# Kernel tuning notes

Measured on AMD Instinct MI355X. Metric: run time of the kernel, lower is better.

The kernel has to match this reference:

```python
import jax, jax.numpy as jnp
import numpy as np

B, N, C, F = 8, 2048, 256, 128

def setup_inputs() -> dict:
    key = jax.random.key(0)
    ks = jax.random.split(key, 5)
    s = 0.02
    return {
        "x": jax.random.normal(ks[0], (B, N, C), dtype=jnp.float32),
        "Wf": jax.random.normal(ks[1], (C, F), dtype=jnp.float32) * s,
        "bf": jnp.zeros((F,), jnp.float32),
        "Wg": jax.random.normal(ks[2], (C, F), dtype=jnp.float32) * s,
        "bg": jnp.zeros((F,), jnp.float32),
        "Wh": jax.random.normal(ks[3], (C, F), dtype=jnp.float32) * s,
        "bh": jnp.zeros((F,), jnp.float32),
        "Wv": jax.random.normal(ks[4], (F, F), dtype=jnp.float32) * s,
        "bv": jnp.zeros((F,), jnp.float32),
    }

def reference(x, Wf, bf, Wg, bg, Wh, bh, Wv, bv):
    # 1x1 Conv1D == pointwise dense projection
    fx = x @ Wf + bf            # [B, N, F]
    gx = x @ Wg + bg            # [B, N, F]
    hx = x @ Wh + bh            # [B, N, F]
    # alpha = softmax(fx @ gx^T) over last axis -> [B, N, N]
    alpha = jax.nn.softmax(jnp.einsum('bnf,bmf->bnm', fx, gx), axis=-1)
    # o = hx^T @ alpha -> [B, F, N]
    o = jnp.einsum('bnf,bnm->bfm', hx, alpha)
    # faithful to original: RESHAPE (not transpose) to [B, N, F]
    o = o.reshape(B, N, F)
    return o @ Wv + bv          # [B, N, F]
```

## Files before the change

kernel.cpp:

```cpp
#include <hip/hip_runtime.h>
#include <hip/hip_bf16.h>


constexpr int Bb = 8, Nn = 2048, Cc = 256, Ff = 128;
constexpr long BNF = (long)Bb * Nn * Ff;
constexpr long BN  = (long)Bb * Nn;

typedef __bf16 bf16x8 __attribute__((ext_vector_type(8)));
typedef float  f32x4  __attribute__((ext_vector_type(4)));

__device__ inline unsigned short f2bf(float x) {
    unsigned u = __float_as_uint(x);
    unsigned r = (u + 0x7fffu + ((u >> 16) & 1u)) >> 16;
    return (unsigned short)r;
}
__device__ inline float bf2f(unsigned short h) {
    return __uint_as_float(((unsigned)h) << 16);
}


__global__ __launch_bounds__(256) void k_prepw(
    const float* __restrict__ W0, const float* __restrict__ W1,
    const float* __restrict__ W2,
    ushort* __restrict__ wth, ushort* __restrict__ wtl)
{
    __shared__ float ls[64][132];
    const float* W = (blockIdx.y == 0) ? W0 : (blockIdx.y == 1) ? W1 : W2;
    const int k0 = blockIdx.x * 64;
    const int t = threadIdx.x;
    const float4* src = (const float4*)(W + (size_t)k0 * 128);
    #pragma unroll
    for (int i = 0; i < 8; ++i) {
        int idx = t + 256 * i;
        int r = idx >> 5, c4 = idx & 31;
        *(float4*)&ls[r][c4 * 4] = src[idx];
    }
    __syncthreads();
    const int f = t >> 1, half = t & 1;
    __align__(16) ushort hb[32], lb[32];
    #pragma unroll
    for (int j = 0; j < 32; ++j) {
        float v = ls[half * 32 + j][f];
        ushort h = f2bf(v);
        hb[j] = h;
        lb[j] = f2bf(v - bf2f(h));
    }
    size_t base = ((size_t)blockIdx.y * 128 + f) * 256 + k0 + half * 32;
    #pragma unroll
    for (int j = 0; j < 4; ++j) {
        *(uint4*)&wth[base + j * 8] = *(const uint4*)&hb[j * 8];
        *(uint4*)&wtl[base + j * 8] = *(const uint4*)&lb[j * 8];
    }
}

__global__ __launch_bounds__(256) void k_prepwv(
    const float* __restrict__ Wv,
    ushort* __restrict__ wvth, ushort* __restrict__ wvtl)
{
    __shared__ float ls[64][132];
    const int k0 = blockIdx.x * 64;
    const int t = threadIdx.x;
    const float4* src = (const float4*)(Wv + (size_t)k0 * 128);
    #pragma unroll
    for (int i = 0; i < 8; ++i) {
        int idx = t + 256 * i;
        int r = idx >> 5, c4 = idx & 31;
        *(float4*)&ls[r][c4 * 4] = src[idx];
    }
    __syncthreads();
    const int f = t >> 1, half = t & 1;
    __align__(16) ushort hb[32], lb[32];
    #pragma unroll
    for (int j = 0; j < 32; ++j) {
        float v = ls[half * 32 + j][f];
        ushort h = f2bf(v);
        hb[j] = h;
        lb[j] = f2bf(v - bf2f(h));
    }
    size_t base = (size_t)f * 128 + k0 + half * 32;
    #pragma unroll
    for (int j = 0; j < 4; ++j) {
        *(uint4*)&wvth[base + j * 8] = *(const uint4*)&hb[j * 8];
        *(uint4*)&wvtl[base + j * 8] = *(const uint4*)&lb[j * 8];
    }
}

__global__ __launch_bounds__(512) void k_projm2(
    const float* __restrict__ x,
    const ushort* __restrict__ wth, const ushort* __restrict__ wtl,
    const float* __restrict__ b0, const float* __restrict__ b1,
    const float* __restrict__ b2,
    ushort* __restrict__ fxh, ushort* __restrict__ fxl,
    ushort* __restrict__ gxh, ushort* __restrict__ gxl,
    float* __restrict__ hxt)
{
    __shared__ ushort xsh[64][264], xsl[64][264];
    __shared__ float pmf[64][132];
    ushort (*pm)[136] = (ushort(*)[136])pmf;

    const int t = threadIdx.x;
    const long row0 = (long)blockIdx.x * 64;
    const int wid = t >> 6, lane = t & 63;
    const int wy = wid & 1, wx = wid >> 1;
    const int col = lane & 15, quad = lane >> 4;

    {
        #pragma unroll
        for (int i = 0; i < 8; ++i) {
            int idx = t + 512 * i;
            int r = idx >> 6, c4 = idx & 63;
            float4 v = *(const float4*)&x[(row0 + r) * 256 + c4 * 4];
            ushort4 h, l;
            h.x = f2bf(v.x); l.x = f2bf(v.x - bf2f(h.x));
            h.y = f2bf(v.y); l.y = f2bf(v.y - bf2f(h.y));
            h.z = f2bf(v.z); l.z = f2bf(v.z - bf2f(h.z));
            h.w = f2bf(v.w); l.w = f2bf(v.w - bf2f(h.w));
            *(ushort4*)&xsh[r][c4 * 4] = h;
            *(ushort4*)&xsl[r][c4 * 4] = l;
        }
    }
    __syncthreads();

    for (int y = 0; y < 3; ++y) {
        const ushort* Wh = wth + (size_t)y * 128 * 256;
        const ushort* Wl = wtl + (size_t)y * 128 * 256;
        const float* bias = (y == 0) ? b0 : (y == 1) ? b1 : b2;

        f32x4 acc[2][2];
        #pragma unroll
        for (int i = 0; i < 2; ++i)
            #pragma unroll
            for (int j = 0; j < 2; ++j) acc[i][j] = (f32x4){0.f, 0.f, 0.f, 0.f};

        #pragma unroll
        for (int kk = 0; kk < 8; ++kk) {
            const int ko = kk * 32 + quad * 8;
            bf16x8 ah[2], al[2], bh[2], bl[2];
            #pragma unroll
            for (int tn = 0; tn < 2; ++tn) {
                int r = wy * 32 + tn * 16 + col;
                ah[tn] = *(const bf16x8*)&xsh[r][ko];
                al[tn] = *(const bf16x8*)&xsl[r][ko];
            }
            #pragma unroll
            for (int tf = 0; tf < 2; ++tf) {
                int f = wx * 32 + tf * 16 + col;
                bh[tf] = *(const bf16x8*)&Wh[(size_t)f * 256 + ko];
                bl[tf] = *(const bf16x8*)&Wl[(size_t)f * 256 + ko];
            }
            #pragma unroll
            for (int tn = 0; tn < 2; ++tn)
                #pragma unroll
                for (int tf = 0; tf < 2; ++tf) {
                    acc[tn][tf] = __builtin_amdgcn_mfma_f32_16x16x32_bf16(ah[tn], bh[tf], acc[tn][tf], 0, 0, 0);
                    acc[tn][tf] = __builtin_amdgcn_mfma_f32_16x16x32_bf16(ah[tn], bl[tf], acc[tn][tf], 0, 0, 0);
                    acc[tn][tf] = __builtin_amdgcn_mfma_f32_16x16x32_bf16(al[tn], bh[tf], acc[tn][tf], 0, 0, 0);
                }
        }

        float v[2][2][4];
        #pragma unroll
        for (int tf = 0; tf < 2; ++tf) {
            float bb = bias[wx * 32 + tf * 16 + col];
            #pragma unroll
            for (int tn = 0; tn < 2; ++tn)
                #pragma unroll
                for (int r = 0; r < 4; ++r) v[tn][tf][r] = acc[tn][tf][r] + bb;
        }

        if (y == 2) {
            float* ob = hxt + (row0 >> 11) * (size_t)128 * 2048;
            int n0 = (int)(row0 & 2047);
            #pragma unroll
            for (int tn = 0; tn < 2; ++tn) {
                int n = n0 + wy * 32 + tn * 16 + quad * 4;
                #pragma unroll
                for (int tf = 0; tf < 2; ++tf) {
                    int f = wx * 32 + tf * 16 + col;
                    f32x4 vv = {v[tn][tf][0], v[tn][tf][1], v[tn][tf][2], v[tn][tf][3]};
                    *(f32x4*)&ob[(size_t)f * 2048 + n] = vv;
                }
            }
        } else {
            ushort* oh = (y == 0) ? fxh : gxh;
            ushort* ol = (y == 0) ? fxl : gxl;
            __syncthreads();
            #pragma unroll
            for (int tn = 0; tn < 2; ++tn)
                #pragma unroll
                for (int tf = 0; tf < 2; ++tf)
                    #pragma unroll
                    for (int r = 0; r < 4; ++r)
                        pm[wy * 32 + tn * 16 + quad * 4 + r][wx * 32 + tf * 16 + col] = f2bf(v[tn][tf][r]);
            __syncthreads();
            #pragma unroll
            for (int i = 0; i < 2; ++i) {
                int idx = t + 512 * i;
                int r = idx >> 4, c = idx & 15;
                *(uint4*)&oh[(row0 + r) * 128 + c * 8] = *(const uint4*)&pm[r][c * 8];
            }
            __syncthreads();
            #pragma unroll
            for (int tn = 0; tn < 2; ++tn)
                #pragma unroll
                for (int tf = 0; tf < 2; ++tf)
                    #pragma unroll
                    for (int r = 0; r < 4; ++r) {
                        float hv = bf2f(f2bf(v[tn][tf][r]));
                        pm[wy * 32 + tn * 16 + quad * 4 + r][wx * 32 + tf * 16 + col] = f2bf(v[tn][tf][r] - hv);
                    }
            __syncthreads();
            #pragma unroll
            for (int i = 0; i < 2; ++i) {
                int idx = t + 512 * i;
                int r = idx >> 4, c = idx & 15;
                *(uint4*)&ol[(row0 + r) * 128 + c * 8] = *(const uint4*)&pm[r][c * 8];
            }
            __syncthreads();
        }
    }
}

__global__ __launch_bounds__(512, 4) void k_score5(
    const ushort* __restrict__ fxh, const ushort* __restrict__ fxl,
    const ushort* __restrict__ gxh, const ushort* __restrict__ gxl,
    ushort* __restrict__ Pt, float* __restrict__ lsum2)
{
    __shared__ ushort gsh[64][136], gsl[64][136];
    __shared__ __align__(16) ushort fsbuf[2 * 64 * 136];
    __shared__ float lsum[64];
    ushort* fsh = fsbuf;
    ushort* fsl = fsbuf + 64 * 136;
    ushort* pm  = fsbuf;

    const int t = threadIdx.x;
    const int n0g = blockIdx.x * 64;
    const int ms = blockIdx.y;
    const int b = n0g >> 11;
    const int n0 = n0g & 2047;
    const int wid = t >> 6, lane = t & 63;
    const int wy = wid & 1, wx = wid >> 1;
    const int col = lane & 15, quad = lane >> 4;

    {
        const uint4* sh = (const uint4*)(fxh + (size_t)n0g * 128);
        const uint4* sl = (const uint4*)(fxl + (size_t)n0g * 128);
        #pragma unroll
        for (int i = 0; i < 2; ++i) {
            int idx = t + 512 * i;
            int r = idx >> 4, c = idx & 15;
            *(uint4*)&fsh[r * 136 + c * 8] = sh[idx];
            *(uint4*)&fsl[r * 136 + c * 8] = sl[idx];
        }
        if (t < 64) lsum[t] = 0.f;
    }
    __syncthreads();

    bf16x8 Ah[4][2], Al[4][2];
    #pragma unroll
    for (int kk = 0; kk < 4; ++kk) {
        const int ko = kk * 32 + quad * 8;
        #pragma unroll
        for (int tn = 0; tn < 2; ++tn) {
            int r = wy * 32 + tn * 16 + col;
            Ah[kk][tn] = *(const bf16x8*)&fsh[r * 136 + ko];
            Al[kk][tn] = *(const bf16x8*)&fsl[r * 136 + ko];
        }
    }

    float rs[2][4] = {};
    const ushort* gbh = gxh + (size_t)b * 2048 * 128;
    const ushort* gbl = gxl + (size_t)b * 2048 * 128;
    ushort* Pb = Pt + (size_t)b * 2048 * 2048;

    for (int mt = 0; mt < 16; ++mt) {
        const int m0 = ms * 1024 + mt * 64;
        __syncthreads();
        {
            const uint4* sh = (const uint4*)(gbh + (size_t)m0 * 128);
            const uint4* sl = (const uint4*)(gbl + (size_t)m0 * 128);
            #pragma unroll
            for (int i = 0; i < 2; ++i) {
                int idx = t + 512 * i;
                int r = idx >> 4, c = idx & 15;
                *(uint4*)&gsh[r][c * 8] = sh[idx];
                *(uint4*)&gsl[r][c * 8] = sl[idx];
            }
        }
        __syncthreads();

        f32x4 acc[2];
        acc[0] = (f32x4){0.f, 0.f, 0.f, 0.f};
        acc[1] = (f32x4){0.f, 0.f, 0.f, 0.f};

        #pragma unroll
        for (int kk = 0; kk < 4; ++kk) {
            const int ko = kk * 32 + quad * 8;
            int r = wx * 16 + col;
            bf16x8 bh = *(const bf16x8*)&gsh[r][ko];
            bf16x8 bl = *(const bf16x8*)&gsl[r][ko];
            #pragma unroll
            for (int tn = 0; tn < 2; ++tn) {
                acc[tn] = __builtin_amdgcn_mfma_f32_16x16x32_bf16(Ah[kk][tn], bh, acc[tn], 0, 0, 0);
                acc[tn] = __builtin_amdgcn_mfma_f32_16x16x32_bf16(Ah[kk][tn], bl, acc[tn], 0, 0, 0);
                acc[tn] = __builtin_amdgcn_mfma_f32_16x16x32_bf16(Al[kk][tn], bh, acc[tn], 0, 0, 0);
            }
        }

        #pragma unroll
        for (int tn = 0; tn < 2; ++tn) {
            float e0 = __expf(acc[tn][0]);
            float e1 = __expf(acc[tn][1]);
            float e2 = __expf(acc[tn][2]);
            float e3 = __expf(acc[tn][3]);
            rs[tn][0] += e0; rs[tn][1] += e1; rs[tn][2] += e2; rs[tn][3] += e3;
            ushort4 pk;
            pk.x = f2bf(e0); pk.y = f2bf(e1); pk.z = f2bf(e2); pk.w = f2bf(e3);
            int ml = wx * 16 + col;
            int nl = wy * 32 + tn * 16 + quad * 4;
            *(ushort4*)&pm[ml * 72 + nl] = pk;
        }
        __syncthreads();
        {
            int r = t >> 3, c = t & 7;
            *(uint4*)&Pb[(size_t)(m0 + r) * 2048 + n0 + c * 8] = *(const uint4*)&pm[r * 72 + c * 8];
        }
    }

    #pragma unroll
    for (int off = 1; off < 16; off <<= 1)
        #pragma unroll
        for (int tn = 0; tn < 2; ++tn)
            #pragma unroll
            for (int r = 0; r < 4; ++r) rs[tn][r] += __shfl_xor(rs[tn][r], off);
    if (col == 0) {
        #pragma unroll
        for (int tn = 0; tn < 2; ++tn)
            #pragma unroll
            for (int r = 0; r < 4; ++r)
                atomicAdd(&lsum[wy * 32 + tn * 16 + quad * 4 + r], rs[tn][r]);
    }
    __syncthreads();
    if (t < 64) lsum2[(size_t)ms * BN + n0g + t] = lsum[t];
}

__global__ __launch_bounds__(256) void k_scaleh4(
    const float* __restrict__ hxt, const float* __restrict__ lsum2,
    ushort* __restrict__ hth, ushort* __restrict__ htl)
{
    const int t = threadIdx.x;
    const int bf = blockIdx.x;
    const int b = bf >> 7;
    const size_t base = (size_t)bf * 2048;
    const size_t gn = (size_t)b * 2048 + t * 8;
    const int n = t * 8;

    float4 v0 = *(const float4*)&hxt[base + n];
    float4 v1 = *(const float4*)&hxt[base + n + 4];
    float l[8] = {};
    #pragma unroll
    for (int ms = 0; ms < 2; ++ms) {
        float4 a = *(const float4*)&lsum2[(size_t)ms * BN + gn];
        float4 c = *(const float4*)&lsum2[(size_t)ms * BN + gn + 4];
        l[0] += a.x; l[1] += a.y; l[2] += a.z; l[3] += a.w;
        l[4] += c.x; l[5] += c.y; l[6] += c.z; l[7] += c.w;
    }
    float vv[8] = {v0.x, v0.y, v0.z, v0.w, v1.x, v1.y, v1.z, v1.w};
    __align__(16) ushort hb[8], lb[8];
    #pragma unroll
    for (int j = 0; j < 8; ++j) {
        float w = vv[j] * (1.0f / l[j]);
        ushort h = f2bf(w);
        hb[j] = h;
        lb[j] = f2bf(w - bf2f(h));
    }
    *(uint4*)&hth[base + n] = *(const uint4*)&hb[0];
    *(uint4*)&htl[base + n] = *(const uint4*)&lb[0];
}

__global__ __launch_bounds__(256) void k_pv3(
    const ushort* __restrict__ Pt,
    const ushort* __restrict__ hth, const ushort* __restrict__ htl,
    float* __restrict__ op0, float* __restrict__ op1)
{
    __shared__ ushort ps[32][72];
    __shared__ ushort hsh[128][72], hsl[128][72];
    const int t = threadIdx.x;
    const int ks = blockIdx.x & 1;
    const int m0g = (blockIdx.x >> 1) * 32;
    const int b = m0g >> 11, m0 = m0g & 2047;
    const int wx = t >> 6;
    const int lane = t & 63;
    const int col = lane & 15, quad = lane >> 4;
    const int nbase = ks * 1024;

    const ushort* Pb = Pt + ((size_t)b * 2048 + m0) * 2048 + nbase;
    const ushort* Hh = hth + (size_t)b * 128 * 2048 + nbase;
    const ushort* Hl = htl + (size_t)b * 128 * 2048 + nbase;

    f32x4 acc[2][2];
    #pragma unroll
    for (int i = 0; i < 2; ++i)
        #pragma unroll
        for (int j = 0; j < 2; ++j) acc[i][j] = (f32x4){0.f, 0.f, 0.f, 0.f};

    for (int nt = 0; nt < 16; ++nt) {
        __syncthreads();
        {
            int r = t >> 3, c = t & 7;
            *(uint4*)&ps[r][c * 8] = *(const uint4*)&Pb[(size_t)r * 2048 + nt * 64 + c * 8];
            #pragma unroll
            for (int i = 0; i < 4; ++i) {
                int idx = t + 256 * i;
                int rr = idx >> 3, cc = idx & 7;
                size_t g = (size_t)rr * 2048 + nt * 64 + cc * 8;
                *(uint4*)&hsh[rr][cc * 8] = *(const uint4*)&Hh[g];
                *(uint4*)&hsl[rr][cc * 8] = *(const uint4*)&Hl[g];
            }
        }
        __syncthreads();

        #pragma unroll
        for (int kk = 0; kk < 2; ++kk) {
            const int ko = kk * 32 + quad * 8;
            bf16x8 a[2], bh[2], bl[2];
            #pragma unroll
            for (int tm = 0; tm < 2; ++tm)
                a[tm] = *(const bf16x8*)&ps[tm * 16 + col][ko];
            #pragma unroll
            for (int tf = 0; tf < 2; ++tf) {
                int r = wx * 32 + tf * 16 + col;
                bh[tf] = *(const bf16x8*)&hsh[r][ko];
                bl[tf] = *(const bf16x8*)&hsl[r][ko];
            }
            #pragma unroll
            for (int tm = 0; tm < 2; ++tm)
                #pragma unroll
                for (int tf = 0; tf < 2; ++tf) {
                    acc[tm][tf] = __builtin_amdgcn_mfma_f32_16x16x32_bf16(a[tm], bh[tf], acc[tm][tf], 0, 0, 0);
                    acc[tm][tf] = __builtin_amdgcn_mfma_f32_16x16x32_bf16(a[tm], bl[tf], acc[tm][tf], 0, 0, 0);
                }
        }
    }

    float* op = (ks == 0) ? op0 : op1;
    float* ob = op + (size_t)b * 128 * 2048;
    #pragma unroll
    for (int tm = 0; tm < 2; ++tm) {
        int m = m0 + tm * 16 + quad * 4;
        #pragma unroll
        for (int tf = 0; tf < 2; ++tf) {
            int f = wx * 32 + tf * 16 + col;
            *(f32x4*)&ob[(size_t)f * 2048 + m] = acc[tm][tf];
        }
    }
}

__global__ __launch_bounds__(512) void k_final_m2(
    const float* __restrict__ op0, const float* __restrict__ op1,
    const ushort* __restrict__ wvth, const ushort* __restrict__ wvtl,
    const float* __restrict__ bv, float* __restrict__ out)
{
    __shared__ ushort ash[64][136], asl[64][136];
    __shared__ float pmf[64][132];
    const int t = threadIdx.x;
    const long row0 = (long)blockIdx.x * 64;
    const int wid = t >> 6, lane = t & 63;
    const int wy = wid & 1, wx = wid >> 1;
    const int col = lane & 15, quad = lane >> 4;

    {
        const float4* s0 = (const float4*)(op0 + row0 * 128);
        const float4* s1 = (const float4*)(op1 + row0 * 128);
        #pragma unroll
        for (int i = 0; i < 4; ++i) {
            int idx = t + 512 * i;
            float4 a = s0[idx], bq = s1[idx];
            float v0 = a.x + bq.x, v1 = a.y + bq.y, v2 = a.z + bq.z, v3 = a.w + bq.w;
            ushort4 h, l;
            h.x = f2bf(v0); l.x = f2bf(v0 - bf2f(h.x));
            h.y = f2bf(v1); l.y = f2bf(v1 - bf2f(h.y));
            h.z = f2bf(v2); l.z = f2bf(v2 - bf2f(h.z));
            h.w = f2bf(v3); l.w = f2bf(v3 - bf2f(h.w));
            int r = idx >> 5, c4 = idx & 31;
            *(ushort4*)&ash[r][c4 * 4] = h;
            *(ushort4*)&asl[r][c4 * 4] = l;
        }
    }
    __syncthreads();

    f32x4 acc[2][2];
    #pragma unroll
    for (int i = 0; i < 2; ++i)
        #pragma unroll
        for (int j = 0; j < 2; ++j) acc[i][j] = (f32x4){0.f, 0.f, 0.f, 0.f};

    #pragma unroll
    for (int kk = 0; kk < 4; ++kk) {
        const int ko = kk * 32 + quad * 8;
        bf16x8 ah[2], al[2], bh[2], bl[2];
        #pragma unroll
        for (int tn = 0; tn < 2; ++tn) {
            int r = wy * 32 + tn * 16 + col;
            ah[tn] = *(const bf16x8*)&ash[r][ko];
            al[tn] = *(const bf16x8*)&asl[r][ko];
        }
        #pragma unroll
        for (int tf = 0; tf < 2; ++tf) {
            int f = wx * 32 + tf * 16 + col;
            bh[tf] = *(const bf16x8*)&wvth[(size_t)f * 128 + ko];
            bl[tf] = *(const bf16x8*)&wvtl[(size_t)f * 128 + ko];
        }
        #pragma unroll
        for (int tn = 0; tn < 2; ++tn)
            #pragma unroll
            for (int tf = 0; tf < 2; ++tf) {
                acc[tn][tf] = __builtin_amdgcn_mfma_f32_16x16x32_bf16(ah[tn], bh[tf], acc[tn][tf], 0, 0, 0);
                acc[tn][tf] = __builtin_amdgcn_mfma_f32_16x16x32_bf16(ah[tn], bl[tf], acc[tn][tf], 0, 0, 0);
                acc[tn][tf] = __builtin_amdgcn_mfma_f32_16x16x32_bf16(al[tn], bh[tf], acc[tn][tf], 0, 0, 0);
            }
    }

    #pragma unroll
    for (int tf = 0; tf < 2; ++tf) {
        int f = wx * 32 + tf * 16 + col;
        float bb = bv[f];
        #pragma unroll
        for (int tn = 0; tn < 2; ++tn)
            #pragma unroll
            for (int r = 0; r < 4; ++r)
                pmf[wy * 32 + tn * 16 + quad * 4 + r][f] = acc[tn][tf][r] + bb;
    }
    __syncthreads();
    #pragma unroll
    for (int i = 0; i < 4; ++i) {
        int idx = t + 512 * i;
        int r = idx >> 5, c4 = idx & 31;
        *(float4*)&out[(row0 + r) * 128 + c4 * 4] = *(const float4*)&pmf[r][c4 * 4];
    }
}


__global__ __launch_bounds__(256) void k_proj(
    const float* __restrict__ x,
    const float* __restrict__ W0, const float* __restrict__ b0,
    const float* __restrict__ W1, const float* __restrict__ b1,
    const float* __restrict__ W2, const float* __restrict__ b2,
    float* __restrict__ o0, float* __restrict__ o1, float* __restrict__ o2)
{
    const float* W; const float* bias; float* out;
    if (blockIdx.y == 0)      { W = W0; bias = b0; out = o0; }
    else if (blockIdx.y == 1) { W = W1; bias = b1; out = o1; }
    else                      { W = W2; bias = b2; out = o2; }

    __shared__ float xs[32][Cc];
    const int t = threadIdx.x;
    const long row0 = (long)blockIdx.x * 32;
    const float4* xg = (const float4*)(x + row0 * Cc);
    float4* xs4 = (float4*)xs;
    #pragma unroll
    for (int i = 0; i < 8; ++i) xs4[t + 256 * i] = xg[t + 256 * i];
    __syncthreads();

    const int cg = t & 31;
    const int rq = t >> 5;
    float acc[4][4] = {};
    const float4* W4 = (const float4*)W;
    for (int k4 = 0; k4 < Cc / 4; ++k4) {
        float4 av[4];
        #pragma unroll
        for (int i = 0; i < 4; ++i) av[i] = *(const float4*)&xs[4 * rq + i][k4 * 4];
        float4 wv4[4];
        #pragma unroll
        for (int kk = 0; kk < 4; ++kk) wv4[kk] = W4[(size_t)(4 * k4 + kk) * (Ff / 4) + cg];
        #pragma unroll
        for (int kk = 0; kk < 4; ++kk) {
            float4 w = wv4[kk];
            #pragma unroll
            for (int i = 0; i < 4; ++i) {
                float a = (kk == 0) ? av[i].x : (kk == 1) ? av[i].y : (kk == 2) ? av[i].z : av[i].w;
                acc[i][0] += a * w.x; acc[i][1] += a * w.y;
                acc[i][2] += a * w.z; acc[i][3] += a * w.w;
            }
        }
    }
    float4 bb = ((const float4*)bias)[cg];
    #pragma unroll
    for (int i = 0; i < 4; ++i) {
        float4 r;
        r.x = acc[i][0] + bb.x; r.y = acc[i][1] + bb.y;
        r.z = acc[i][2] + bb.z; r.w = acc[i][3] + bb.w;
        ((float4*)(out + (row0 + 4 * rq + i) * Ff))[cg] = r;
    }
}

__global__ __launch_bounds__(256) void k_stats(
    const float* __restrict__ fx, const float* __restrict__ gx,
    float* __restrict__ linv)
{
    __shared__ float fs[64][132];
    __shared__ float gs[128][132];
    const int t = threadIdx.x;
    const int n0 = blockIdx.x * 64;
    const int b = n0 / Nn;
    const float* gxb = gx + (long)b * Nn * Ff;
    {
        const float4* src = (const float4*)(fx + (long)n0 * Ff);
        #pragma unroll
        for (int i = 0; i < 8; ++i) {
            int idx = t + 256 * i;
            int r = idx >> 5, c4 = idx & 31;
            *(float4*)&fs[r][c4 * 4] = src[idx];
        }
    }
    const int ty = t >> 4;
    const int tx = t & 15;
    float lsum[4] = {0.f, 0.f, 0.f, 0.f};
    for (int mt = 0; mt < Nn / 128; ++mt) {
        __syncthreads();
        {
            const float4* src = (const float4*)(gxb + (long)mt * 128 * Ff);
            #pragma unroll
            for (int i = 0; i < 16; ++i) {
                int idx = t + 256 * i;
                int r = idx >> 5, c4 = idx & 31;
                *(float4*)&gs[r][c4 * 4] = src[idx];
            }
        }
        __syncthreads();
        float s[4][8] = {};
        for (int k4 = 0; k4 < 32; ++k4) {
            float4 a[4], g4[8];
            #pragma unroll
            for (int i = 0; i < 4; ++i) a[i] = *(const float4*)&fs[ty + 16 * i][k4 * 4];
            #pragma unroll
            for (int j = 0; j < 8; ++j) g4[j] = *(const float4*)&gs[tx + 16 * j][k4 * 4];
            #pragma unroll
            for (int i = 0; i < 4; ++i)
                #pragma unroll
                for (int j = 0; j < 8; ++j)
                    s[i][j] += a[i].x * g4[j].x + a[i].y * g4[j].y
                             + a[i].z * g4[j].z + a[i].w * g4[j].w;
        }
        #pragma unroll
        for (int i = 0; i < 4; ++i) {
            float e = 0.f;
            #pragma unroll
            for (int j = 0; j < 8; ++j) e += __expf(s[i][j]);
            lsum[i] += e;
        }
    }
    #pragma unroll
    for (int off = 1; off < 16; off <<= 1)
        #pragma unroll
        for (int i = 0; i < 4; ++i) lsum[i] += __shfl_xor(lsum[i], off);
    if (tx == 0)
        #pragma unroll
        for (int i = 0; i < 4; ++i) linv[n0 + ty + 16 * i] = 1.0f / lsum[i];
}

__global__ __launch_bounds__(256) void k_attnpv(
    const float* __restrict__ fx, const float* __restrict__ gx,
    const float* __restrict__ hx, const float* __restrict__ linv,
    float* __restrict__ o)
{
    __shared__ float gs[64][132];
    __shared__ float fs[64][132];
    __shared__ float hs[64][132];
    __shared__ float ps[64][68];
    __shared__ float li[64];
    const int t = threadIdx.x;
    const int m0g = blockIdx.x * 64;
    const int b = m0g / Nn;
    const int m0 = m0g - b * Nn;
    const float* fxb = fx + (long)b * Nn * Ff;
    const float* hxb = hx + (long)b * Nn * Ff;
    {
        const float4* src = (const float4*)(gx + (long)m0g * Ff);
        #pragma unroll
        for (int i = 0; i < 8; ++i) {
            int idx = t + 256 * i;
            int r = idx >> 5, c4 = idx & 31;
            *(float4*)&gs[r][c4 * 4] = src[idx];
        }
    }
    const int ty = t >> 4;
    const int tx = t & 15;
    float acc[4][8] = {};
    for (int nt = 0; nt < Nn / 64; ++nt) {
        __syncthreads();
        {
            const float4* srcf = (const float4*)(fxb + (long)nt * 64 * Ff);
            const float4* srch = (const float4*)(hxb + (long)nt * 64 * Ff);
            #pragma unroll
            for (int i = 0; i < 8; ++i) {
                int idx = t + 256 * i;
                int r = idx >> 5, c4 = idx & 31;
                *(float4*)&fs[r][c4 * 4] = srcf[idx];
                *(float4*)&hs[r][c4 * 4] = srch[idx];
            }
            if (t < 64) li[t] = linv[(long)b * Nn + nt * 64 + t];
        }
        __syncthreads();
        float s[4][4] = {};
        for (int k4 = 0; k4 < 32; ++k4) {
            float4 a[4], g4[4];
            #pragma unroll
            for (int i = 0; i < 4; ++i) a[i] = *(const float4*)&fs[ty + 16 * i][k4 * 4];
            #pragma unroll
            for (int j = 0; j < 4; ++j) g4[j] = *(const float4*)&gs[tx + 16 * j][k4 * 4];
            #pragma unroll
            for (int i = 0; i < 4; ++i)
                #pragma unroll
                for (int j = 0; j < 4; ++j)
                    s[i][j] += a[i].x * g4[j].x + a[i].y * g4[j].y
                             + a[i].z * g4[j].z + a[i].w * g4[j].w;
        }
        #pragma unroll
        for (int i = 0; i < 4; ++i) {
            float lv = li[ty + 16 * i];
            #pragma unroll
            for (int j = 0; j < 4; ++j)
                ps[ty + 16 * i][tx + 16 * j] = __expf(s[i][j]) * lv;
        }
        __syncthreads();
        #pragma unroll 4
        for (int n = 0; n < 64; ++n) {
            float4 h0 = *(const float4*)&hs[n][tx * 8];
            float4 h1 = *(const float4*)&hs[n][tx * 8 + 4];
            float pv[4];
            #pragma unroll
            for (int im = 0; im < 4; ++im) pv[im] = ps[n][ty + 16 * im];
            #pragma unroll
            for (int im = 0; im < 4; ++im) {
                acc[im][0] += pv[im] * h0.x; acc[im][1] += pv[im] * h0.y;
                acc[im][2] += pv[im] * h0.z; acc[im][3] += pv[im] * h0.w;
                acc[im][4] += pv[im] * h1.x; acc[im][5] += pv[im] * h1.y;
                acc[im][6] += pv[im] * h1.z; acc[im][7] += pv[im] * h1.w;
            }
        }
    }
    float* ob = o + (size_t)b * Ff * Nn;
    #pragma unroll
    for (int im = 0; im < 4; ++im) {
        int m = m0 + ty + 16 * im;
        #pragma unroll
        for (int jf = 0; jf < 8; ++jf)
            ob[(size_t)(tx * 8 + jf) * Nn + m] = acc[im][jf];
    }
}

__global__ __launch_bounds__(256) void k_final(
    const float* __restrict__ in2, const float* __restrict__ Wv,
    const float* __restrict__ bv, float* __restrict__ out)
{
    __shared__ float xs[32][132];
    const int t = threadIdx.x;
    const long row0 = (long)blockIdx.x * 32;
    {
        const float4* src = (const float4*)(in2 + row0 * Ff);
        #pragma unroll
        for (int i = 0; i < 4; ++i) {
            int idx = t + 256 * i;
            int r = idx >> 5, c4 = idx & 31;
            *(float4*)&xs[r][c4 * 4] = src[idx];
        }
    }
    __syncthreads();

    const int cg = t & 31;
    const int rq = t >> 5;
    float acc[4][4] = {};
    const float4* W4 = (const float4*)Wv;
    for (int k4 = 0; k4 < 32; ++k4) {
        float4 av[4];
        #pragma unroll
        for (int i = 0; i < 4; ++i) av[i] = *(const float4*)&xs[4 * rq + i][k4 * 4];
        float4 wv4[4];
        #pragma unroll
        for (int kk = 0; kk < 4; ++kk) wv4[kk] = W4[(size_t)(4 * k4 + kk) * 32 + cg];
        #pragma unroll
        for (int kk = 0; kk < 4; ++kk) {
            float4 w = wv4[kk];
            #pragma unroll
            for (int i = 0; i < 4; ++i) {
                float a = (kk == 0) ? av[i].x : (kk == 1) ? av[i].y : (kk == 2) ? av[i].z : av[i].w;
                acc[i][0] += a * w.x; acc[i][1] += a * w.y;
                acc[i][2] += a * w.z; acc[i][3] += a * w.w;
            }
        }
    }
    float4 bb = ((const float4*)bv)[cg];
    #pragma unroll
    for (int i = 0; i < 4; ++i) {
        float4 r;
        r.x = acc[i][0] + bb.x; r.y = acc[i][1] + bb.y;
        r.z = acc[i][2] + bb.z; r.w = acc[i][3] + bb.w;
        ((float4*)(out + (row0 + 4 * rq + i) * Ff))[cg] = r;
    }
}


extern "C" void kernel_launch(void* const* d_in, const int* in_sizes, int n_in,
                              void* d_out, int out_size, void* d_ws, size_t ws_size,
                              hipStream_t stream) {
    const float* x  = (const float*)d_in[0];
    const float* Wf = (const float*)d_in[1];
    const float* bf = (const float*)d_in[2];
    const float* Wg = (const float*)d_in[3];
    const float* bg = (const float*)d_in[4];
    const float* Wh = (const float*)d_in[5];
    const float* bh = (const float*)d_in[6];
    const float* Wv = (const float*)d_in[7];
    const float* bv = (const float*)d_in[8];
    float* out = (float*)d_out;

    const size_t sz_hxt  = (size_t)BNF * 4;
    const size_t sz_linv = (size_t)BN * 4;
    const size_t sz_bf   = (size_t)BNF * 2;
    const size_t sz_Pt   = (size_t)Bb * Nn * Nn * 2;
    const size_t sz_wt   = (size_t)3 * 128 * 256 * 2;
    const size_t sz_wv   = (size_t)128 * 128 * 2;
    const size_t need = sz_hxt + sz_linv + 8 * sz_bf + sz_Pt + 2 * sz_wt + 2 * sz_wv;

    if (ws_size >= need) {
        char* p = (char*)d_ws;
        float* hxt   = (float*)p;            p += sz_hxt;
        p += sz_linv;
        ushort* fxh  = (ushort*)p;           p += sz_bf;
        ushort* fxl  = (ushort*)p;           p += sz_bf;
        ushort* gxh  = (ushort*)p;           p += sz_bf;
        ushort* gxl  = (ushort*)p;           p += sz_bf;
        ushort* hth  = (ushort*)p;           p += sz_bf;
        ushort* htl  = (ushort*)p;           p += sz_bf;
        float* lsum2 = (float*)p;
        float* op0   = hxt;
        float* op1   = (float*)fxh;
        p += 2 * sz_bf;
        ushort* wth  = (ushort*)p;           p += sz_wt;
        ushort* wtl  = (ushort*)p;           p += sz_wt;
        ushort* wvth = (ushort*)p;           p += sz_wv;
        ushort* wvtl = (ushort*)p;           p += sz_wv;
        ushort* Pt   = (ushort*)p;

        k_prepw   <<<dim3(4, 3), 256, 0, stream>>>(Wf, Wg, Wh, wth, wtl);
        k_prepwv  <<<2, 256, 0, stream>>>(Wv, wvth, wvtl);
        k_projm2  <<<BN / 64, 512, 0, stream>>>(x, wth, wtl, bf, bg, bh,
                                                fxh, fxl, gxh, gxl, hxt);
        k_score5  <<<dim3(BN / 64, 2), 512, 0, stream>>>(fxh, fxl, gxh, gxl, Pt, lsum2);
        k_scaleh4 <<<Bb * Ff, 256, 0, stream>>>(hxt, lsum2, hth, htl);
        k_pv3     <<<(BN / 32) * 2, 256, 0, stream>>>(Pt, hth, htl, op0, op1);
        k_final_m2<<<BN / 64, 512, 0, stream>>>(op0, op1, wvth, wvtl, bv, out);
    } else {
        float* ws   = (float*)d_ws;
        float* fx   = ws;
        float* gx   = fx + BNF;
        float* hx   = gx + BNF;
        float* linv = hx + BNF;
        float* o    = linv + BN;
        k_proj  <<<dim3(BN / 32, 3), 256, 0, stream>>>(x, Wf, bf, Wg, bg, Wh, bh, fx, gx, hx);
        k_stats <<<BN / 64, 256, 0, stream>>>(fx, gx, linv);
        k_attnpv<<<BN / 64, 256, 0, stream>>>(fx, gx, hx, linv, o);
        k_final <<<BN / 32, 256, 0, stream>>>(o, Wv, bv, out);
    }
}
```

Baseline: 195.4 us.

## Register-prefetch next tiles in score and PV kernels; enlarge PV row tile

Both the score kernel and the P·V kernel now load the next iteration's global tiles into registers while MFMAs run on the current shared-memory tile. This hides global load latency and drops one barrier per iteration. The PV kernel also doubles its row tile from 32 to 64, so each staged H tile is reused across twice as many rows and half as many blocks are launched. The cost is more live registers, which may reduce occupancy, and fewer blocks in the PV grid.

```diff
diff --git a/kernel.cpp b/kernel.cpp
--- a/kernel.cpp
+++ b/kernel.cpp
@@ -221,7 +221,7 @@
     }
 }
 
-__global__ __launch_bounds__(512, 4) void k_score5(
+__global__ __launch_bounds__(512, 4) void k_score6(
     const ushort* __restrict__ fxh, const ushort* __restrict__ fxl,
     const ushort* __restrict__ gxh, const ushort* __restrict__ gxl,
     ushort* __restrict__ Pt, float* __restrict__ lsum2)
@@ -273,21 +273,33 @@
     const ushort* gbl = gxl + (size_t)b * 2048 * 128;
     ushort* Pb = Pt + (size_t)b * 2048 * 2048;
 
+    const int sr0 = t >> 4, sc0 = t & 15;
+    const int sr1 = (t + 512) >> 4, sc1 = (t + 512) & 15;
+
+    uint4 grh[2], grl[2];
+    {
+        const size_t m0 = (size_t)(ms * 1024) * 128;
+        grh[0] = *(const uint4*)&gbh[m0 + (size_t)sr0 * 128 + sc0 * 8];
+        grl[0] = *(const uint4*)&gbl[m0 + (size_t)sr0 * 128 + sc0 * 8];
+        grh[1] = *(const uint4*)&gbh[m0 + (size_t)sr1 * 128 + sc1 * 8];
+        grl[1] = *(const uint4*)&gbl[m0 + (size_t)sr1 * 128 + sc1 * 8];
+    }
+
     for (int mt = 0; mt < 16; ++mt) {
         const int m0 = ms * 1024 + mt * 64;
+        *(uint4*)&gsh[sr0][sc0 * 8] = grh[0];
+        *(uint4*)&gsl[sr0][sc0 * 8] = grl[0];
+        *(uint4*)&gsh[sr1][sc1 * 8] = grh[1];
+        *(uint4*)&gsl[sr1][sc1 * 8] = grl[1];
         __syncthreads();
-        {
-            const uint4* sh = (const uint4*)(gbh + (size_t)m0 * 128);
-            const uint4* sl = (const uint4*)(gbl + (size_t)m0 * 128);
-            #pragma unroll
-            for (int i = 0; i < 2; ++i) {
-                int idx = t + 512 * i;
-                int r = idx >> 4, c = idx & 15;
-                *(uint4*)&gsh[r][c * 8] = sh[idx];
-                *(uint4*)&gsl[r][c * 8] = sl[idx];
-            }
-        }
-        __syncthreads();
+
+        if (mt + 1 < 16) {
+            const size_t mo = (size_t)(ms * 1024 + (mt + 1) * 64) * 128;
+            grh[0] = *(const uint4*)&gbh[mo + (size_t)sr0 * 128 + sc0 * 8];
+            grl[0] = *(const uint4*)&gbl[mo + (size_t)sr0 * 128 + sc0 * 8];
+            grh[1] = *(const uint4*)&gbh[mo + (size_t)sr1 * 128 + sc1 * 8];
+            grl[1] = *(const uint4*)&gbl[mo + (size_t)sr1 * 128 + sc1 * 8];
+        }
 
         f32x4 acc[2];
         acc[0] = (f32x4){0.f, 0.f, 0.f, 0.f};
@@ -378,16 +390,16 @@
     *(uint4*)&htl[base + n] = *(const uint4*)&lb[0];
 }
 
-__global__ __launch_bounds__(256) void k_pv3(
+__global__ __launch_bounds__(256) void k_pv6(
     const ushort* __restrict__ Pt,
     const ushort* __restrict__ hth, const ushort* __restrict__ htl,
     float* __restrict__ op0, float* __restrict__ op1)
 {
-    __shared__ ushort ps[32][72];
+    __shared__ ushort ps[64][72];
     __shared__ ushort hsh[128][72], hsl[128][72];
     const int t = threadIdx.x;
     const int ks = blockIdx.x & 1;
-    const int m0g = (blockIdx.x >> 1) * 32;
+    const int m0g = (blockIdx.x >> 1) * 64;
     const int b = m0g >> 11, m0 = m0g & 2047;
     const int wx = t >> 6;
     const int lane = t & 63;
@@ -398,34 +410,70 @@
     const ushort* Hh = hth + (size_t)b * 128 * 2048 + nbase;
     const ushort* Hl = htl + (size_t)b * 128 * 2048 + nbase;
 
-    f32x4 acc[2][2];
-    #pragma unroll
-    for (int i = 0; i < 2; ++i)
+    uint4 pr[2], hrh[4], hrl[4];
+    {
+        #pragma unroll
+        for (int i = 0; i < 2; ++i) {
+            int idx = t + 256 * i;
+            int r = idx >> 3, c = idx & 7;
+            pr[i] = *(const uint4*)&Pb[(size_t)r * 2048 + c * 8];
+        }
+        #pragma unroll
+        for (int i = 0; i < 4; ++i) {
+            int idx = t + 256 * i;
+            int r = idx >> 3, c = idx & 7;
+            size_t g = (size_t)r * 2048 + c * 8;
+            hrh[i] = *(const uint4*)&Hh[g];
+            hrl[i] = *(const uint4*)&Hl[g];
+        }
+    }
+
+    f32x4 acc[4][2];
+    #pragma unroll
+    for (int i = 0; i < 4; ++i)
         #pragma unroll
         for (int j = 0; j < 2; ++j) acc[i][j] = (f32x4){0.f, 0.f, 0.f, 0.f};
 
     for (int nt = 0; nt < 16; ++nt) {
+        #pragma unroll
+        for (int i = 0; i < 2; ++i) {
+            int idx = t + 256 * i;
+            int r = idx >> 3, c = idx & 7;
+            *(uint4*)&ps[r][c * 8] = pr[i];
+        }
+        #pragma unroll
+        for (int i = 0; i < 4; ++i) {
+            int idx = t + 256 * i;
+            int r = idx >> 3, c = idx & 7;
+            *(uint4*)&hsh[r][c * 8] = hrh[i];
+            *(uint4*)&hsl[r][c * 8] = hrl[i];
+        }
         __syncthreads();
-        {
-            int r = t >> 3, c = t & 7;
-            *(uint4*)&ps[r][c * 8] = *(const uint4*)&Pb[(size_t)r * 2048 + nt * 64 + c * 8];
+
+        if (nt + 1 < 16) {
+            const size_t no = (size_t)(nt + 1) * 64;
+            #pragma unroll
+            for (int i = 0; i < 2; ++i) {
+                int idx = t + 256 * i;
+                int r = idx >> 3, c = idx & 7;
+                pr[i] = *(const uint4*)&Pb[(size_t)r * 2048 + no + c * 8];
+            }
             #pragma unroll
             for (int i = 0; i < 4; ++i) {
                 int idx = t + 256 * i;
-                int rr = idx >> 3, cc = idx & 7;
-                size_t g = (size_t)rr * 2048 + nt * 64 + cc * 8;
-                *(uint4*)&hsh[rr][cc * 8] = *(const uint4*)&Hh[g];
-                *(uint4*)&hsl[rr][cc * 8] = *(const uint4*)&Hl[g];
-            }
-        }
-        __syncthreads();
+                int r = idx >> 3, c = idx & 7;
+                size_t g = (size_t)r * 2048 + no + c * 8;
+                hrh[i] = *(const uint4*)&Hh[g];
+                hrl[i] = *(const uint4*)&Hl[g];
+            }
+        }
 
         #pragma unroll
         for (int kk = 0; kk < 2; ++kk) {
             const int ko = kk * 32 + quad * 8;
-            bf16x8 a[2], bh[2], bl[2];
-            #pragma unroll
-            for (int tm = 0; tm < 2; ++tm)
+            bf16x8 a[4], bh[2], bl[2];
+            #pragma unroll
+            for (int tm = 0; tm < 4; ++tm)
                 a[tm] = *(const bf16x8*)&ps[tm * 16 + col][ko];
             #pragma unroll
             for (int tf = 0; tf < 2; ++tf) {
@@ -434,19 +482,20 @@
                 bl[tf] = *(const bf16x8*)&hsl[r][ko];
             }
             #pragma unroll
-            for (int tm = 0; tm < 2; ++tm)
+            for (int tm = 0; tm < 4; ++tm)
                 #pragma unroll
                 for (int tf = 0; tf < 2; ++tf) {
                     acc[tm][tf] = __builtin_amdgcn_mfma_f32_16x16x32_bf16(a[tm], bh[tf], acc[tm][tf], 0, 0, 0);
                     acc[tm][tf] = __builtin_amdgcn_mfma_f32_16x16x32_bf16(a[tm], bl[tf], acc[tm][tf], 0, 0, 0);
                 }
         }
+        __syncthreads();
     }
 
     float* op = (ks == 0) ? op0 : op1;
     float* ob = op + (size_t)b * 128 * 2048;
     #pragma unroll
-    for (int tm = 0; tm < 2; ++tm) {
+    for (int tm = 0; tm < 4; ++tm) {
         int m = m0 + tm * 16 + quad * 4;
         #pragma unroll
         for (int tf = 0; tf < 2; ++tf) {
@@ -847,9 +896,9 @@
         k_prepwv  <<<2, 256, 0, stream>>>(Wv, wvth, wvtl);
         k_projm2  <<<BN / 64, 512, 0, stream>>>(x, wth, wtl, bf, bg, bh,
                                                 fxh, fxl, gxh, gxl, hxt);
-        k_score5  <<<dim3(BN / 64, 2), 512, 0, stream>>>(fxh, fxl, gxh, gxl, Pt, lsum2);
+        k_score6  <<<dim3(BN / 64, 2), 512, 0, stream>>>(fxh, fxl, gxh, gxl, Pt, lsum2);
         k_scaleh4 <<<Bb * Ff, 256, 0, stream>>>(hxt, lsum2, hth, htl);
-        k_pv3     <<<(BN / 32) * 2, 256, 0, stream>>>(Pt, hth, htl, op0, op1);
+        k_pv6     <<<(BN / 64) * 2, 256, 0, stream>>>(Pt, hth, htl, op0, op1);
         k_final_m2<<<BN / 64, 512, 0, stream>>>(op0, op1, wvth, wvtl, bv, out);
     } else {
         float* ws   = (float*)d_ws;
```

Result: slower. 320.2 us (+63.8%).

## Enlarge PV tile to 128 rows with 4-way split-K over sequence

Applied to the files above, without the earlier changes.

The P·H kernel now computes 128 output rows per block instead of 32, so each staged tile of scaled H (high and low bf16 parts) is reused across four times as many rows. To keep enough blocks in flight, the key dimension is split four ways, and the four partial results go into reused workspace buffers. The final projection kernel sums all four partials. This cuts redundant H loads, at the cost of more accumulator registers per thread and extra partial-sum traffic in the final kernel.

```diff
diff --git a/kernel.cpp b/kernel.cpp
--- a/kernel.cpp
+++ b/kernel.cpp
@@ -378,44 +378,44 @@
     *(uint4*)&htl[base + n] = *(const uint4*)&lb[0];
 }
 
-__global__ __launch_bounds__(256) void k_pv3(
+__global__ __launch_bounds__(256, 2) void k_pv7(
     const ushort* __restrict__ Pt,
     const ushort* __restrict__ hth, const ushort* __restrict__ htl,
-    float* __restrict__ op0, float* __restrict__ op1)
-{
-    __shared__ ushort ps[32][72];
+    float* __restrict__ op0, float* __restrict__ op1,
+    float* __restrict__ op2, float* __restrict__ op3)
+{
+    __shared__ ushort ps[128][72];
     __shared__ ushort hsh[128][72], hsl[128][72];
     const int t = threadIdx.x;
-    const int ks = blockIdx.x & 1;
-    const int m0g = (blockIdx.x >> 1) * 32;
+    const int ks = blockIdx.x & 3;
+    const int m0g = (blockIdx.x >> 2) * 128;
     const int b = m0g >> 11, m0 = m0g & 2047;
     const int wx = t >> 6;
     const int lane = t & 63;
     const int col = lane & 15, quad = lane >> 4;
-    const int nbase = ks * 1024;
+    const int nbase = ks * 512;
 
     const ushort* Pb = Pt + ((size_t)b * 2048 + m0) * 2048 + nbase;
     const ushort* Hh = hth + (size_t)b * 128 * 2048 + nbase;
     const ushort* Hl = htl + (size_t)b * 128 * 2048 + nbase;
 
-    f32x4 acc[2][2];
-    #pragma unroll
-    for (int i = 0; i < 2; ++i)
+    f32x4 acc[8][2];
+    #pragma unroll
+    for (int i = 0; i < 8; ++i)
         #pragma unroll
         for (int j = 0; j < 2; ++j) acc[i][j] = (f32x4){0.f, 0.f, 0.f, 0.f};
 
-    for (int nt = 0; nt < 16; ++nt) {
+    for (int nt = 0; nt < 8; ++nt) {
         __syncthreads();
         {
-            int r = t >> 3, c = t & 7;
-            *(uint4*)&ps[r][c * 8] = *(const uint4*)&Pb[(size_t)r * 2048 + nt * 64 + c * 8];
             #pragma unroll
             for (int i = 0; i < 4; ++i) {
                 int idx = t + 256 * i;
-                int rr = idx >> 3, cc = idx & 7;
-                size_t g = (size_t)rr * 2048 + nt * 64 + cc * 8;
-                *(uint4*)&hsh[rr][cc * 8] = *(const uint4*)&Hh[g];
-                *(uint4*)&hsl[rr][cc * 8] = *(const uint4*)&Hl[g];
+                int r = idx >> 3, c = idx & 7;
+                size_t g = (size_t)r * 2048 + nt * 64 + c * 8;
+                *(uint4*)&ps[r][c * 8]  = *(const uint4*)&Pb[g];
+                *(uint4*)&hsh[r][c * 8] = *(const uint4*)&Hh[g];
+                *(uint4*)&hsl[r][c * 8] = *(const uint4*)&Hl[g];
             }
         }
         __syncthreads();
@@ -423,9 +423,9 @@
         #pragma unroll
         for (int kk = 0; kk < 2; ++kk) {
             const int ko = kk * 32 + quad * 8;
-            bf16x8 a[2], bh[2], bl[2];
-            #pragma unroll
-            for (int tm = 0; tm < 2; ++tm)
+            bf16x8 a[8], bh[2], bl[2];
+            #pragma unroll
+            for (int tm = 0; tm < 8; ++tm)
                 a[tm] = *(const bf16x8*)&ps[tm * 16 + col][ko];
             #pragma unroll
             for (int tf = 0; tf < 2; ++tf) {
@@ -434,7 +434,7 @@
                 bl[tf] = *(const bf16x8*)&hsl[r][ko];
             }
             #pragma unroll
-            for (int tm = 0; tm < 2; ++tm)
+            for (int tm = 0; tm < 8; ++tm)
                 #pragma unroll
                 for (int tf = 0; tf < 2; ++tf) {
                     acc[tm][tf] = __builtin_amdgcn_mfma_f32_16x16x32_bf16(a[tm], bh[tf], acc[tm][tf], 0, 0, 0);
@@ -443,10 +443,10 @@
         }
     }
 
-    float* op = (ks == 0) ? op0 : op1;
+    float* op = (ks == 0) ? op0 : (ks == 1) ? op1 : (ks == 2) ? op2 : op3;
     float* ob = op + (size_t)b * 128 * 2048;
     #pragma unroll
-    for (int tm = 0; tm < 2; ++tm) {
+    for (int tm = 0; tm < 8; ++tm) {
         int m = m0 + tm * 16 + quad * 4;
         #pragma unroll
         for (int tf = 0; tf < 2; ++tf) {
@@ -456,8 +456,9 @@
     }
 }
 
-__global__ __launch_bounds__(512) void k_final_m2(
+__global__ __launch_bounds__(512) void k_final_m3(
     const float* __restrict__ op0, const float* __restrict__ op1,
+    const float* __restrict__ op2, const float* __restrict__ op3,
     const ushort* __restrict__ wvth, const ushort* __restrict__ wvtl,
     const float* __restrict__ bv, float* __restrict__ out)
 {
@@ -472,11 +473,16 @@
     {
         const float4* s0 = (const float4*)(op0 + row0 * 128);
         const float4* s1 = (const float4*)(op1 + row0 * 128);
+        const float4* s2 = (const float4*)(op2 + row0 * 128);
+        const float4* s3 = (const float4*)(op3 + row0 * 128);
         #pragma unroll
         for (int i = 0; i < 4; ++i) {
             int idx = t + 512 * i;
-            float4 a = s0[idx], bq = s1[idx];
-            float v0 = a.x + bq.x, v1 = a.y + bq.y, v2 = a.z + bq.z, v3 = a.w + bq.w;
+            float4 a = s0[idx], bq = s1[idx], cq = s2[idx], dq = s3[idx];
+            float v0 = ((a.x + bq.x) + cq.x) + dq.x;
+            float v1 = ((a.y + bq.y) + cq.y) + dq.y;
+            float v2 = ((a.z + bq.z) + cq.z) + dq.z;
+            float v3 = ((a.w + bq.w) + cq.w) + dq.w;
             ushort4 h, l;
             h.x = f2bf(v0); l.x = f2bf(v0 - bf2f(h.x));
             h.y = f2bf(v1); l.y = f2bf(v1 - bf2f(h.y));
@@ -834,8 +840,10 @@
         ushort* hth  = (ushort*)p;           p += sz_bf;
         ushort* htl  = (ushort*)p;           p += sz_bf;
         float* lsum2 = (float*)p;
+        float* op3   = (float*)p;
         float* op0   = hxt;
         float* op1   = (float*)fxh;
+        float* op2   = (float*)gxh;
         p += 2 * sz_bf;
         ushort* wth  = (ushort*)p;           p += sz_wt;
         ushort* wtl  = (ushort*)p;           p += sz_wt;
@@ -849,8 +857,8 @@
                                                 fxh, fxl, gxh, gxl, hxt);
         k_score5  <<<dim3(BN / 64, 2), 512, 0, stream>>>(fxh, fxl, gxh, gxl, Pt, lsum2);
         k_scaleh4 <<<Bb * Ff, 256, 0, stream>>>(hxt, lsum2, hth, htl);
-        k_pv3     <<<(BN / 32) * 2, 256, 0, stream>>>(Pt, hth, htl, op0, op1);
-        k_final_m2<<<BN / 64, 512, 0, stream>>>(op0, op1, wvth, wvtl, bv, out);
+        k_pv7     <<<(BN / 128) * 4, 256, 0, stream>>>(Pt, hth, htl, op0, op1, op2, op3);
+        k_final_m3<<<BN / 64, 512, 0, stream>>>(op0, op1, op2, op3, wvth, wvtl, bv, out);
     } else {
         float* ws   = (float*)d_ws;
         float* fx   = ws;
```

Result: faster. 187.6 us (-4.0%).
